# Optimization experiments

Hardware: AMD Instinct MI355X
Metric: run time of the kernel (lower is better)

The kernel has to match this reference:

```python
import jax, jax.numpy as jnp
import numpy as np

DEPTH = 2
DIM = 64
INNER = 256  # hard-coded inner_dim in Attention
HEADS = 1
N = 4096
B = 2
EPS = 1e-5


def layernorm(x, g, b):
    m = jnp.mean(x, axis=-1, keepdims=True)
    v = jnp.var(x, axis=-1, keepdims=True)
    return (x - m) * jax.lax.rsqrt(v + EPS) * g + b


def setup_inputs() -> dict:
    key = jax.random.key(0)
    ks = jax.random.split(key, 16)
    embed = jax.random.normal(ks[0], (B, N, DIM), dtype=jnp.float32)
    A = jax.random.randint(ks[1], (1, HEADS, N, N), 0, 2).astype(jnp.float32)
    s = 0.02
    return {
        "embed": embed,
        "A": A,
        "g1": jnp.ones((DEPTH, DIM), jnp.float32),
        "b1": jnp.zeros((DEPTH, DIM), jnp.float32),
        "Wqkv": jax.random.normal(ks[2], (DEPTH, DIM, INNER * 3), jnp.float32) * s,
        "Wout": jax.random.normal(ks[3], (DEPTH, INNER, DIM), jnp.float32) * s,
        "bout": jnp.zeros((DEPTH, DIM), jnp.float32),
        "g2": jnp.ones((DEPTH, DIM), jnp.float32),
        "b2": jnp.zeros((DEPTH, DIM), jnp.float32),
        "W1": jax.random.normal(ks[4], (DEPTH, DIM, DIM), jnp.float32) * s,
        "bb1": jnp.zeros((DEPTH, DIM), jnp.float32),
        "W2": jax.random.normal(ks[5], (DEPTH, DIM, DIM), jnp.float32) * s,
        "bb2": jnp.zeros((DEPTH, DIM), jnp.float32),
        "gf": jnp.ones((DIM,), jnp.float32),
        "bf": jnp.zeros((DIM,), jnp.float32),
    }


def _encoder(embed, A, g1, b1, Wqkv, Wout, bout, g2, b2, W1, bb1, W2, bb2, gf, bf):
    b, n, dim = embed.shape
    scale = dim ** (-0.5)
    dh = INNER // HEADS
    x = embed
    attn = None
    dots_softmax = None
    diag = jnp.arange(n)
    for l in range(DEPTH):
        xn = layernorm(x, g1[l], b1[l])
        qkv = xn @ Wqkv[l]  # [b, n, 3*INNER]
        q, k, v = jnp.split(qkv, 3, axis=-1)
        # [b, n, INNER] -> [b, h, n, dh]
        q = q.reshape(b, n, HEADS, dh).transpose(0, 2, 1, 3)
        k = k.reshape(b, n, HEADS, dh).transpose(0, 2, 1, 3)
        v = v.reshape(b, n, HEADS, dh).transpose(0, 2, 1, 3)
        dots = jnp.einsum("bhid,bhjd->bhij", q, k) * scale
        dots_softmax = jax.nn.softmax(dots[0, 0], axis=-1)
        # adjacency mask, then only [0][0] kept; diagonal filled with literal 1.0;
        # the original does a cpu/numpy roundtrip with .detach() -> stop_gradient.
        e = jnp.where(A > 0, dots, jnp.float32(-9e15))[0, 0]  # [n, n]
        e = e.at[diag, diag].set(1.0)
        e = jax.lax.stop_gradient(e)
        attn = jax.nn.softmax(e, axis=-1)  # [n, n], shared across b, h
        out = jnp.einsum("ij,bhjd->bhid", attn, v)  # broadcast attn over b,h
        out = out.transpose(0, 2, 1, 3).reshape(b, n, INNER)
        out = out @ Wout[l] + bout[l]
        x = xn + out  # residual onto the NORMED input (as in original)
        xm = layernorm(x, g2[l], b2[l])
        mlp = jax.nn.gelu(xm @ W1[l] + bb1[l], approximate=False) @ W2[l] + bb2[l]
        x = xm + mlp
    x = layernorm(x, gf, bf)
    return x, attn.reshape(1, 1, n, n), dots_softmax


def reference(embed, A, g1, b1, Wqkv, Wout, bout, g2, b2, W1, bb1, W2, bb2, gf, bf):
    return _encoder(embed, A, g1, b1, Wqkv, Wout, bout, g2, b2, W1, bb1, W2, bb2, gf, bf)
```

## Files before the change

### kernel.cpp

```cpp
#include <hip/hip_runtime.h>
#include <hip/hip_bf16.h>
#include <math.h>

typedef __attribute__((ext_vector_type(8))) short short8;
typedef __attribute__((ext_vector_type(4))) float f32x4;

#define NG 16

__device__ __forceinline__ unsigned short f2bf(float x) {
    __hip_bfloat16 b = __float2bfloat16(x);
    return *reinterpret_cast<unsigned short*>(&b);
}
__device__ __forceinline__ float bf2f(unsigned short u) {
    unsigned int t = ((unsigned int)u) << 16;
    float f;
    __builtin_memcpy(&f, &t, 4);
    return f;
}
__device__ __forceinline__ float gelu_exact(float x) {
    return 0.5f * x * (1.0f + erff(x * 0.70710678118654752f));
}

__global__ __launch_bounds__(256) void k_zero(float* __restrict__ p, long n)
{
    long i = (long)blockIdx.x * 256 + threadIdx.x;
    if (i < n) p[i] = 0.f;
}

__global__ __launch_bounds__(256) void k_prologue(
    const float* __restrict__ Aadj, unsigned long long* __restrict__ mask,
    const float* __restrict__ Wqkv, const float* __restrict__ Wout,
    float* __restrict__ Wfold,
    const float* __restrict__ embed, const float* __restrict__ g1,
    const float* __restrict__ b1, float* __restrict__ xn,
    float* __restrict__ zbuf)
{
    int bx = blockIdx.x, tid = threadIdx.x;
    if (bx < 4096) {
        if (!mask) return;
        int row = bx;
        int wave = tid >> 6, lane = tid & 63;
        for (int w = wave; w < 64; w += 4) {
            float a = Aadj[(long)row * 4096 + w * 64 + lane];
            unsigned long long m = __ballot(a > 0.f);
            if (lane == 0) mask[(long)row * 64 + w] = m;
        }
    } else if (bx < 4128) {
        int bid = bx - 4096;
        int l = bid >> 4;
        int idx = (bid & 15) * 256 + tid;
        int c = idx >> 6, d = idx & 63;
        const float* Wq = Wqkv + (long)l * 64 * 768;
        const float* Wo = Wout + (long)l * 256 * 64;
        float a = 0.f;
        for (int k = 0; k < 256; ++k)
            a += Wq[c * 768 + 512 + k] * Wo[k * 64 + d];
        Wfold[l * 4096 + idx] = a;
    } else if (bx < 6176) {
        int wave = tid >> 6, lane = tid & 63;
        long row = (long)(bx - 4128) * 4 + wave;
        float v = embed[row * 64 + lane];
        float s = v;
        #pragma unroll
        for (int o = 32; o; o >>= 1) s += __shfl_xor(s, o);
        float m = s * (1.0f / 64.0f);
        float d = v - m;
        float q = d * d;
        #pragma unroll
        for (int o = 32; o; o >>= 1) q += __shfl_xor(q, o);
        float rstd = rsqrtf(q * (1.0f / 64.0f) + 1e-5f);
        xn[row * 64 + lane] = d * rstd * g1[lane] + b1[lane];
    } else {
        long i = (long)(bx - 6176) * 256 + tid;
        if (i < 524288) zbuf[i] = 0.f;
    }
}

__global__ __launch_bounds__(256) void k_qkx(
    const float* __restrict__ xn, const float* __restrict__ W,
    const float* __restrict__ Wfold,
    unsigned short* __restrict__ q, unsigned short* __restrict__ kmat,
    unsigned short* __restrict__ vWT)
{
    __shared__ float As[64][65];
    __shared__ float Ws[64][65];
    int tid = threadIdx.x;
    int by = blockIdx.y;
    int tx = tid & 15, ty = tid >> 4;
    if (by < 8) {
        int m0 = blockIdx.x * 64, n0 = by * 64;
        #pragma unroll
        for (int it = 0; it < 16; ++it) {
            int idx = tid + it * 256;
            int r = idx >> 6, c = idx & 63;
            As[r][c] = xn[(long)(m0 + r) * 64 + c];
            Ws[r][c] = W[(long)r * 768 + n0 + c];
        }
        __syncthreads();
        float acc[4][4] = {};
        #pragma unroll
        for (int k = 0; k < 64; ++k) {
            float a[4], w[4];
            #pragma unroll
            for (int i = 0; i < 4; ++i) a[i] = As[ty * 4 + i][k];
            #pragma unroll
            for (int j = 0; j < 4; ++j) w[j] = Ws[k][tx * 4 + j];
            #pragma unroll
            for (int i = 0; i < 4; ++i)
                #pragma unroll
                for (int j = 0; j < 4; ++j) acc[i][j] += a[i] * w[j];
        }
        #pragma unroll
        for (int i = 0; i < 4; ++i) {
            long row = m0 + ty * 4 + i;
            #pragma unroll
            for (int j = 0; j < 4; ++j) {
                int col = n0 + tx * 4 + j;
                if (col < 256) q[row * 256 + col] = f2bf(acc[i][j]);
                else           kmat[row * 256 + (col - 256)] = f2bf(acc[i][j]);
            }
        }
    } else {
        int n0 = blockIdx.x * 64, b = by - 8;
        #pragma unroll
        for (int it = 0; it < 16; ++it) {
            int idx = tid + it * 256;
            int r = idx >> 6, c = idx & 63;
            As[r][c] = xn[((long)b * 4096 + n0 + r) * 64 + c];
            Ws[r][c] = Wfold[r * 64 + c];
        }
        __syncthreads();
        float acc[4][4] = {};
        #pragma unroll
        for (int k = 0; k < 64; ++k) {
            float a[4], w[4];
            #pragma unroll
            for (int i = 0; i < 4; ++i) a[i] = As[ty * 4 + i][k];
            #pragma unroll
            for (int j = 0; j < 4; ++j) w[j] = Ws[k][tx * 4 + j];
            #pragma unroll
            for (int i = 0; i < 4; ++i)
                #pragma unroll
                for (int j = 0; j < 4; ++j) acc[i][j] += a[i] * w[j];
        }
        #pragma unroll
        for (int i = 0; i < 4; ++i)
            #pragma unroll
            for (int j = 0; j < 4; ++j)
                vWT[((long)b * 64 + tx * 4 + j) * 4096 + n0 + ty * 4 + i] = f2bf(acc[i][j]);
    }
}

__global__ __launch_bounds__(256) void k_flash(
    const unsigned short* __restrict__ q, const unsigned short* __restrict__ kmat,
    const unsigned short* __restrict__ vwt,
    const unsigned long long* __restrict__ mask, const float* __restrict__ Aadj,
    unsigned short* __restrict__ part,
    float* __restrict__ stats)
{
    __shared__ __align__(16) unsigned short Qs[128 * 64];
    __shared__ __align__(16) unsigned short Ks[128 * 64];
    __shared__ __align__(16) unsigned short Ps[128 * 128];
    int tid = threadIdx.x;
    int lane = tid & 63, wq = tid >> 6;
    int fr = lane & 15, quad = lane >> 4;
    int m0 = blockIdx.x * 128;
    int g  = blockIdx.y;

    f32x4 accO[2][8];
    #pragma unroll
    for (int i = 0; i < 2; ++i)
        #pragma unroll
        for (int j = 0; j < 8; ++j) accO[i][j] = (f32x4){0.f, 0.f, 0.f, 0.f};
    float m_run[2] = {-1e30f, -1e30f};
    float s_run[2] = {0.f, 0.f};

    for (int jt = 0; jt < 2; ++jt) {
        int jb = g * 256 + jt * 128;
        f32x4 accS[8][2];
        #pragma unroll
        for (int i = 0; i < 8; ++i)
            #pragma unroll
            for (int n = 0; n < 2; ++n) accS[i][n] = (f32x4){0.f, 0.f, 0.f, 0.f};
        for (int k0 = 0; k0 < 256; k0 += 64) {
            #pragma unroll
            for (int it = 0; it < 4; ++it) {
                int idx = tid + it * 256;
                int r = idx >> 3, c8 = (idx & 7) * 8;
                *(short8*)&Qs[idx * 8] = *(const short8*)(q    + (long)(m0 + r) * 256 + k0 + c8);
                *(short8*)&Ks[idx * 8] = *(const short8*)(kmat + (long)(jb + r) * 256 + k0 + c8);
            }
            __syncthreads();
            #pragma unroll
            for (int ks = 0; ks < 2; ++ks) {
                short8 ka[8], qb[2];
                #pragma unroll
                for (int i = 0; i < 8; ++i)
                    ka[i] = *(const short8*)&Ks[(i * 16 + fr) * 64 + ks * 32 + quad * 8];
                #pragma unroll
                for (int n = 0; n < 2; ++n)
                    qb[n] = *(const short8*)&Qs[(wq * 32 + n * 16 + fr) * 64 + ks * 32 + quad * 8];
                #pragma unroll
                for (int i = 0; i < 8; ++i)
                    #pragma unroll
                    for (int n = 0; n < 2; ++n)
                        accS[i][n] = __builtin_amdgcn_mfma_f32_16x16x32_bf16(
                            ka[i], qb[n], accS[i][n], 0, 0, 0);
            }
            __syncthreads();
        }
        float al[2];
        #pragma unroll
        for (int n = 0; n < 2; ++n) {
            int qrow = m0 + wq * 32 + n * 16 + fr;
            unsigned long long mw0 = 0, mw1 = 0;
            if (mask) {
                mw0 = mask[(long)qrow * 64 + (jb >> 6)];
                mw1 = mask[(long)qrow * 64 + (jb >> 6) + 1];
            }
            float tm = -1e30f;
            #pragma unroll
            for (int i = 0; i < 8; ++i) {
                #pragma unroll
                for (int r = 0; r < 4; ++r) {
                    int jl = i * 16 + quad * 4 + r;
                    float v = accS[i][n][r] * 0.125f;
                    bool keep = mask ? (((jl < 64 ? (mw0 >> jl) : (mw1 >> (jl - 64))) & 1ull) != 0)
                                     : (Aadj[(long)qrow * 4096 + jb + jl] > 0.f);
                    v = keep ? v : -1e30f;
                    if (jb + jl == qrow) v = 1.0f;
                    accS[i][n][r] = v;
                    tm = fmaxf(tm, v);
                }
            }
            tm = fmaxf(tm, __shfl_xor(tm, 16));
            tm = fmaxf(tm, __shfl_xor(tm, 32));
            float mnew = fmaxf(fmaxf(m_run[n], tm), -1e20f);
            al[n] = __expf(m_run[n] - mnew);
            m_run[n] = mnew;
            float ts = 0.f;
            int qrl = wq * 32 + n * 16 + fr;
            #pragma unroll
            for (int i = 0; i < 8; ++i) {
                float p0 = __expf(accS[i][n][0] - mnew);
                float p1 = __expf(accS[i][n][1] - mnew);
                float p2 = __expf(accS[i][n][2] - mnew);
                float p3 = __expf(accS[i][n][3] - mnew);
                ts += (p0 + p1) + (p2 + p3);
                unsigned int lo = (unsigned int)f2bf(p0) | ((unsigned int)f2bf(p1) << 16);
                unsigned int hi = (unsigned int)f2bf(p2) | ((unsigned int)f2bf(p3) << 16);
                int u = (qrl * 128 + i * 16 + quad * 4) ^ ((fr & 7) << 3);
                *(uint2*)&Ps[u] = make_uint2(lo, hi);
            }
            ts += __shfl_xor(ts, 16);
            ts += __shfl_xor(ts, 32);
            s_run[n] = s_run[n] * al[n] + ts;
        }
        #pragma unroll
        for (int ii = 0; ii < 2; ++ii) {
            float av[4];
            #pragma unroll
            for (int r = 0; r < 4; ++r) av[r] = __shfl(al[ii], quad * 4 + r);
            #pragma unroll
            for (int nn = 0; nn < 8; ++nn)
                #pragma unroll
                for (int r = 0; r < 4; ++r) accO[ii][nn][r] *= av[r];
        }
        #pragma unroll
        for (int it = 0; it < 4; ++it) {
            int idx = tid + it * 256;
            int r = idx >> 3, c8 = (idx & 7) * 8;
            *(short8*)&Qs[idx * 8] = *(const short8*)(vwt + (long)r * 4096 + jb + c8);
            *(short8*)&Ks[idx * 8] = *(const short8*)(vwt + (long)r * 4096 + jb + 64 + c8);
        }
        __syncthreads();
        #pragma unroll
        for (int ks4 = 0; ks4 < 4; ++ks4) {
            const unsigned short* buf = (ks4 < 2) ? Qs : Ks;
            int ksl = ks4 & 1;
            short8 pa[2], vb[8];
            #pragma unroll
            for (int ii = 0; ii < 2; ++ii) {
                int u = ((wq * 32 + ii * 16 + fr) * 128 + ks4 * 32 + quad * 8) ^ ((fr & 7) << 3);
                pa[ii] = *(const short8*)&Ps[u];
            }
            #pragma unroll
            for (int nn = 0; nn < 8; ++nn)
                vb[nn] = *(const short8*)&buf[(nn * 16 + fr) * 64 + ksl * 32 + quad * 8];
            #pragma unroll
            for (int ii = 0; ii < 2; ++ii)
                #pragma unroll
                for (int nn = 0; nn < 8; ++nn)
                    accO[ii][nn] = __builtin_amdgcn_mfma_f32_16x16x32_bf16(
                        pa[ii], vb[nn], accO[ii][nn], 0, 0, 0);
        }
        __syncthreads();
    }
    #pragma unroll
    for (int ii = 0; ii < 2; ++ii) {
        #pragma unroll
        for (int nn = 0; nn < 8; ++nn) {
            int ch = nn * 16 + fr;
            long rowb = m0 + wq * 32 + ii * 16 + quad * 4;
            #pragma unroll
            for (int r = 0; r < 4; ++r)
                part[((long)g * 4096 + rowb + r) * 128 + ch] = f2bf(accO[ii][nn][r]);
        }
    }
    if (quad == 0) {
        #pragma unroll
        for (int n = 0; n < 2; ++n) {
            int qrow = m0 + wq * 32 + n * 16 + fr;
            stats[((long)g * 4096 + qrow) * 2]     = m_run[n];
            stats[((long)g * 4096 + qrow) * 2 + 1] = s_run[n];
        }
    }
}

__global__ __launch_bounds__(256) void k_stats(
    const unsigned short* __restrict__ q, const unsigned short* __restrict__ kmat,
    const unsigned long long* __restrict__ mask, const float* __restrict__ Aadj,
    float* __restrict__ stats2)
{
    __shared__ __align__(16) unsigned short Qs[128 * 64];
    __shared__ __align__(16) unsigned short Ks[128 * 64];
    int tid = threadIdx.x;
    int lane = tid & 63, wq = tid >> 6;
    int fr = lane & 15, quad = lane >> 4;
    int m0 = blockIdx.x * 128;
    int g  = blockIdx.y;
    float m1[2] = {-1e30f, -1e30f}, s1[2] = {0.f, 0.f};
    float m2[2] = {-1e30f, -1e30f}, s2[2] = {0.f, 0.f};

    for (int jt = 0; jt < 2; ++jt) {
        int jb = g * 256 + jt * 128;
        f32x4 accS[8][2];
        #pragma unroll
        for (int i = 0; i < 8; ++i)
            #pragma unroll
            for (int n = 0; n < 2; ++n) accS[i][n] = (f32x4){0.f, 0.f, 0.f, 0.f};
        for (int k0 = 0; k0 < 256; k0 += 64) {
            #pragma unroll
            for (int it = 0; it < 4; ++it) {
                int idx = tid + it * 256;
                int r = idx >> 3, c8 = (idx & 7) * 8;
                *(short8*)&Qs[idx * 8] = *(const short8*)(q    + (long)(m0 + r) * 256 + k0 + c8);
                *(short8*)&Ks[idx * 8] = *(const short8*)(kmat + (long)(jb + r) * 256 + k0 + c8);
            }
            __syncthreads();
            #pragma unroll
            for (int ks = 0; ks < 2; ++ks) {
                short8 ka[8], qb[2];
                #pragma unroll
                for (int i = 0; i < 8; ++i)
                    ka[i] = *(const short8*)&Ks[(i * 16 + fr) * 64 + ks * 32 + quad * 8];
                #pragma unroll
                for (int n = 0; n < 2; ++n)
                    qb[n] = *(const short8*)&Qs[(wq * 32 + n * 16 + fr) * 64 + ks * 32 + quad * 8];
                #pragma unroll
                for (int i = 0; i < 8; ++i)
                    #pragma unroll
                    for (int n = 0; n < 2; ++n)
                        accS[i][n] = __builtin_amdgcn_mfma_f32_16x16x32_bf16(
                            ka[i], qb[n], accS[i][n], 0, 0, 0);
            }
            __syncthreads();
        }
        #pragma unroll
        for (int n = 0; n < 2; ++n) {
            int qrow = m0 + wq * 32 + n * 16 + fr;
            unsigned long long mw0 = 0, mw1 = 0;
            if (mask) {
                mw0 = mask[(long)qrow * 64 + (jb >> 6)];
                mw1 = mask[(long)qrow * 64 + (jb >> 6) + 1];
            }
            float tm1 = -1e30f, tm2 = -1e30f;
            #pragma unroll
            for (int i = 0; i < 8; ++i) {
                #pragma unroll
                for (int r = 0; r < 4; ++r) {
                    int jl = i * 16 + quad * 4 + r;
                    float v = accS[i][n][r] * 0.125f;
                    accS[i][n][r] = v;
                    tm2 = fmaxf(tm2, v);
                    bool keep = mask ? (((jl < 64 ? (mw0 >> jl) : (mw1 >> (jl - 64))) & 1ull) != 0)
                                     : (Aadj[(long)qrow * 4096 + jb + jl] > 0.f);
                    float mv = keep ? v : -1e30f;
                    if (jb + jl == qrow) mv = 1.0f;
                    tm1 = fmaxf(tm1, mv);
                }
            }
            tm1 = fmaxf(tm1, __shfl_xor(tm1, 16));
            tm1 = fmaxf(tm1, __shfl_xor(tm1, 32));
            tm2 = fmaxf(tm2, __shfl_xor(tm2, 16));
            tm2 = fmaxf(tm2, __shfl_xor(tm2, 32));
            float mn1 = fmaxf(fmaxf(m1[n], tm1), -1e20f);
            float mn2 = fmaxf(fmaxf(m2[n], tm2), -1e20f);
            float a1 = __expf(m1[n] - mn1), a2 = __expf(m2[n] - mn2);
            float ts1 = 0.f, ts2 = 0.f;
            #pragma unroll
            for (int i = 0; i < 8; ++i) {
                #pragma unroll
                for (int r = 0; r < 4; ++r) {
                    int jl = i * 16 + quad * 4 + r;
                    float v = accS[i][n][r];
                    ts2 += __expf(v - mn2);
                    bool keep = mask ? (((jl < 64 ? (mw0 >> jl) : (mw1 >> (jl - 64))) & 1ull) != 0)
                                     : (Aadj[(long)qrow * 4096 + jb + jl] > 0.f);
                    float mv = keep ? v : -1e30f;
                    if (jb + jl == qrow) mv = 1.0f;
                    ts1 += __expf(mv - mn1);
                }
            }
            ts1 += __shfl_xor(ts1, 16); ts1 += __shfl_xor(ts1, 32);
            ts2 += __shfl_xor(ts2, 16); ts2 += __shfl_xor(ts2, 32);
            s1[n] = s1[n] * a1 + ts1; m1[n] = mn1;
            s2[n] = s2[n] * a2 + ts2; m2[n] = mn2;
        }
    }
    if (quad == 0) {
        #pragma unroll
        for (int n = 0; n < 2; ++n) {
            int qrow = m0 + wq * 32 + n * 16 + fr;
            *(float4*)&stats2[(long)qrow * 64 + g * 4] =
                make_float4(m1[n], s1[n], m2[n], s2[n]);
        }
    }
}

__global__ __launch_bounds__(256) void k_attn_ds(
    const unsigned short* __restrict__ q, const unsigned short* __restrict__ kmat,
    const unsigned long long* __restrict__ mask, const float* __restrict__ Aadj,
    const float* __restrict__ stats2,
    float* __restrict__ attn, float* __restrict__ ds)
{
    __shared__ __align__(16) unsigned short Qs[128 * 64];
    __shared__ __align__(16) unsigned short Ks[128 * 64];
    int tid = threadIdx.x;
    int lane = tid & 63, wq = tid >> 6;
    int fr = lane & 15, quad = lane >> 4;
    int m0 = blockIdx.x * 128;
    int g  = blockIdx.y;

    float M1[2], S1i[2], M2[2], S2i[2];
    #pragma unroll
    for (int n = 0; n < 2; ++n) {
        int qrow = m0 + wq * 32 + n * 16 + fr;
        float mm1 = -1e30f, mm2 = -1e30f;
        for (int gg = 0; gg < NG; ++gg) {
            float4 s4 = *(const float4*)&stats2[(long)qrow * 64 + gg * 4];
            mm1 = fmaxf(mm1, s4.x);
            mm2 = fmaxf(mm2, s4.z);
        }
        float ss1 = 0.f, ss2 = 0.f;
        for (int gg = 0; gg < NG; ++gg) {
            float4 s4 = *(const float4*)&stats2[(long)qrow * 64 + gg * 4];
            ss1 += s4.y * __expf(s4.x - mm1);
            ss2 += s4.w * __expf(s4.z - mm2);
        }
        M1[n] = mm1; S1i[n] = 1.0f / ss1;
        M2[n] = mm2; S2i[n] = 1.0f / ss2;
    }

    for (int jt = 0; jt < 2; ++jt) {
        int jb = g * 256 + jt * 128;
        f32x4 accS[8][2];
        #pragma unroll
        for (int i = 0; i < 8; ++i)
            #pragma unroll
            for (int n = 0; n < 2; ++n) accS[i][n] = (f32x4){0.f, 0.f, 0.f, 0.f};
        for (int k0 = 0; k0 < 256; k0 += 64) {
            #pragma unroll
            for (int it = 0; it < 4; ++it) {
                int idx = tid + it * 256;
                int r = idx >> 3, c8 = (idx & 7) * 8;
                *(short8*)&Qs[idx * 8] = *(const short8*)(q    + (long)(m0 + r) * 256 + k0 + c8);
                *(short8*)&Ks[idx * 8] = *(const short8*)(kmat + (long)(jb + r) * 256 + k0 + c8);
            }
            __syncthreads();
            #pragma unroll
            for (int ks = 0; ks < 2; ++ks) {
                short8 ka[8], qb[2];
                #pragma unroll
                for (int i = 0; i < 8; ++i)
                    ka[i] = *(const short8*)&Ks[(i * 16 + fr) * 64 + ks * 32 + quad * 8];
                #pragma unroll
                for (int n = 0; n < 2; ++n)
                    qb[n] = *(const short8*)&Qs[(wq * 32 + n * 16 + fr) * 64 + ks * 32 + quad * 8];
                #pragma unroll
                for (int i = 0; i < 8; ++i)
                    #pragma unroll
                    for (int n = 0; n < 2; ++n)
                        accS[i][n] = __builtin_amdgcn_mfma_f32_16x16x32_bf16(
                            ka[i], qb[n], accS[i][n], 0, 0, 0);
            }
            __syncthreads();
        }
        #pragma unroll
        for (int n = 0; n < 2; ++n) {
            int qrow = m0 + wq * 32 + n * 16 + fr;
            unsigned long long mw0 = 0, mw1 = 0;
            if (mask) {
                mw0 = mask[(long)qrow * 64 + (jb >> 6)];
                mw1 = mask[(long)qrow * 64 + (jb >> 6) + 1];
            }
            #pragma unroll
            for (int i = 0; i < 8; ++i) {
                float4 du, da;
                float* dup = &du.x; float* dap = &da.x;
                #pragma unroll
                for (int r = 0; r < 4; ++r) {
                    int jl = i * 16 + quad * 4 + r;
                    float v = accS[i][n][r] * 0.125f;
                    dup[r] = __expf(v - M2[n]) * S2i[n];
                    bool keep = mask ? (((jl < 64 ? (mw0 >> jl) : (mw1 >> (jl - 64))) & 1ull) != 0)
                                     : (Aadj[(long)qrow * 4096 + jb + jl] > 0.f);
                    float mv = keep ? v : -1e30f;
                    if (jb + jl == qrow) mv = 1.0f;
                    dap[r] = __expf(mv - M1[n]) * S1i[n];
                }
                long off = (long)qrow * 4096 + jb + i * 16 + quad * 4;
                *(float4*)&ds[off]   = du;
                *(float4*)&attn[off] = da;
            }
        }
    }
}

__global__ __launch_bounds__(256) void k_mfma_splitk(
    const float* __restrict__ A, const unsigned short* __restrict__ B,
    float* __restrict__ C)
{
    __shared__ __align__(16) unsigned short As[128 * 64];
    __shared__ __align__(16) unsigned short Bs[128 * 64];
    const int K = 4096, N = 128;
    int tid = threadIdx.x;
    int lane = tid & 63, wave = tid >> 6;
    long m0 = (long)blockIdx.x * 128;
    int k0base = blockIdx.y * 512;
    const float* Ag = A + m0 * K;
    int wm = (wave & 1) * 64, wn = (wave >> 1) * 64;
    int fr = lane & 15, quad = lane >> 4;

    f32x4 acc[4][4];
    #pragma unroll
    for (int i = 0; i < 4; ++i)
        #pragma unroll
        for (int j = 0; j < 4; ++j) acc[i][j] = (f32x4){0.f, 0.f, 0.f, 0.f};

    for (int k0 = k0base; k0 < k0base + 512; k0 += 64) {
        #pragma unroll
        for (int it = 0; it < 4; ++it) {
            int c = tid + it * 256;
            int r = c >> 3, col = (c & 7) * 8;
            float4 f0 = *(const float4*)(Ag + (long)r * K + k0 + col);
            float4 f1 = *(const float4*)(Ag + (long)r * K + k0 + col + 4);
            short8 s;
            s[0] = (short)f2bf(f0.x); s[1] = (short)f2bf(f0.y);
            s[2] = (short)f2bf(f0.z); s[3] = (short)f2bf(f0.w);
            s[4] = (short)f2bf(f1.x); s[5] = (short)f2bf(f1.y);
            s[6] = (short)f2bf(f1.z); s[7] = (short)f2bf(f1.w);
            *(short8*)&As[c * 8] = s;
            *(short8*)&Bs[c * 8] = *(const short8*)(B + (long)r * K + k0 + col);
        }
        __syncthreads();
        #pragma unroll
        for (int ks = 0; ks < 2; ++ks) {
            short8 af[4], bfr[4];
            #pragma unroll
            for (int i = 0; i < 4; ++i) {
                af[i]  = *(const short8*)&As[(wm + i * 16 + fr) * 64 + ks * 32 + quad * 8];
                bfr[i] = *(const short8*)&Bs[(wn + i * 16 + fr) * 64 + ks * 32 + quad * 8];
            }
            #pragma unroll
            for (int i = 0; i < 4; ++i)
                #pragma unroll
                for (int j = 0; j < 4; ++j)
                    acc[i][j] = __builtin_amdgcn_mfma_f32_16x16x32_bf16(
                        af[i], bfr[j], acc[i][j], 0, 0, 0);
        }
        __syncthreads();
    }
    #pragma unroll
    for (int i = 0; i < 4; ++i) {
        #pragma unroll
        for (int j = 0; j < 4; ++j) {
            long col = wn + j * 16 + fr;
            long rowb = m0 + wm + i * 16 + quad * 4;
            #pragma unroll
            for (int r = 0; r < 4; ++r)
                atomicAdd(&C[(rowb + r) * N + col], acc[i][j][r]);
        }
    }
}

__global__ __launch_bounds__(256) void k_mlp(
    int mode, const float* __restrict__ xn,
    const unsigned short* __restrict__ part, const float* __restrict__ fstats,
    const float* __restrict__ avcat, const float* __restrict__ boutv,
    const float* __restrict__ gin, const float* __restrict__ bin,
    const float* __restrict__ W1, const float* __restrict__ bb1,
    const float* __restrict__ W2, const float* __restrict__ bb2,
    const float* __restrict__ gout, const float* __restrict__ bln,
    float* __restrict__ out)
{
    __shared__ float As[64][65];
    __shared__ float W1s[64][65];
    __shared__ float W2s[64][65];
    __shared__ float wg[64][NG];
    int tid = threadIdx.x;
    int m0 = blockIdx.x * 64;
    if (mode == 0 && tid < 64) {
        int n = (m0 + tid) & 4095;
        float mg[NG], sg[NG];
        float mx = -1e30f;
        #pragma unroll
        for (int g = 0; g < NG; ++g) {
            mg[g] = fstats[((long)g * 4096 + n) * 2];
            sg[g] = fstats[((long)g * 4096 + n) * 2 + 1];
            mx = fmaxf(mx, mg[g]);
        }
        float stot = 0.f;
        float w[NG];
        #pragma unroll
        for (int g = 0; g < NG; ++g) { w[g] = __expf(mg[g] - mx); stot += w[g] * sg[g]; }
        float inv = 1.0f / stot;
        #pragma unroll
        for (int g = 0; g < NG; ++g) wg[tid][g] = w[g] * inv;
    }
    __syncthreads();
    #pragma unroll
    for (int it = 0; it < 16; ++it) {
        int idx = tid + it * 256;
        int r = idx >> 6, c = idx & 63;
        long row = m0 + r;
        int n = (int)(row & 4095), bb = (int)(row >> 12);
        float v = xn[row * 64 + c] + boutv[c];
        if (mode == 0) {
            #pragma unroll
            for (int g = 0; g < NG; ++g)
                v += wg[r][g] * bf2f(part[((long)g * 4096 + n) * 128 + bb * 64 + c]);
        } else {
            v += avcat[(long)n * 128 + bb * 64 + c];
        }
        As[r][c]  = v;
        W1s[r][c] = W1[(long)r * 64 + c];
        W2s[r][c] = W2[(long)r * 64 + c];
    }
    __syncthreads();
    int tx = tid & 15, ty = tid >> 4;
    #pragma unroll
    for (int i = 0; i < 4; ++i) {
        float vv[4];
        float s = 0.f;
        #pragma unroll
        for (int j = 0; j < 4; ++j) { vv[j] = As[ty * 4 + i][tx * 4 + j]; s += vv[j]; }
        #pragma unroll
        for (int o = 1; o < 16; o <<= 1) s += __shfl_xor(s, o);
        float m = s * (1.0f / 64.0f);
        float qv = 0.f;
        #pragma unroll
        for (int j = 0; j < 4; ++j) { float d = vv[j] - m; qv += d * d; }
        #pragma unroll
        for (int o = 1; o < 16; o <<= 1) qv += __shfl_xor(qv, o);
        float rstd = rsqrtf(qv * (1.0f / 64.0f) + 1e-5f);
        #pragma unroll
        for (int j = 0; j < 4; ++j) {
            int col = tx * 4 + j;
            As[ty * 4 + i][col] = (vv[j] - m) * rstd * gin[col] + bin[col];
        }
    }
    __syncthreads();
    float acc[4][4] = {};
    #pragma unroll
    for (int k = 0; k < 64; ++k) {
        float a[4], w[4];
        #pragma unroll
        for (int i = 0; i < 4; ++i) a[i] = As[ty * 4 + i][k];
        #pragma unroll
        for (int j = 0; j < 4; ++j) w[j] = W1s[k][tx * 4 + j];
        #pragma unroll
        for (int i = 0; i < 4; ++i)
            #pragma unroll
            for (int j = 0; j < 4; ++j) acc[i][j] += a[i] * w[j];
    }
    __syncthreads();
    #pragma unroll
    for (int i = 0; i < 4; ++i)
        #pragma unroll
        for (int j = 0; j < 4; ++j)
            W1s[ty * 4 + i][tx * 4 + j] = gelu_exact(acc[i][j] + bb1[tx * 4 + j]);
    __syncthreads();
    float acc2[4][4] = {};
    #pragma unroll
    for (int k = 0; k < 64; ++k) {
        float a[4], w[4];
        #pragma unroll
        for (int i = 0; i < 4; ++i) a[i] = W1s[ty * 4 + i][k];
        #pragma unroll
        for (int j = 0; j < 4; ++j) w[j] = W2s[k][tx * 4 + j];
        #pragma unroll
        for (int i = 0; i < 4; ++i)
            #pragma unroll
            for (int j = 0; j < 4; ++j) acc2[i][j] += a[i] * w[j];
    }
    #pragma unroll
    for (int i = 0; i < 4; ++i) {
        float v[4];
        float s = 0.f;
        #pragma unroll
        for (int j = 0; j < 4; ++j) {
            v[j] = acc2[i][j] + bb2[tx * 4 + j] + As[ty * 4 + i][tx * 4 + j];
            s += v[j];
        }
        #pragma unroll
        for (int o = 1; o < 16; o <<= 1) s += __shfl_xor(s, o);
        float m = s * (1.0f / 64.0f);
        float qv = 0.f;
        #pragma unroll
        for (int j = 0; j < 4; ++j) { float d = v[j] - m; qv += d * d; }
        #pragma unroll
        for (int o = 1; o < 16; o <<= 1) qv += __shfl_xor(qv, o);
        float rstd = rsqrtf(qv * (1.0f / 64.0f) + 1e-5f);
        long row = m0 + ty * 4 + i;
        #pragma unroll
        for (int j = 0; j < 4; ++j) {
            int col = tx * 4 + j;
            out[row * 64 + col] = (v[j] - m) * rstd * gout[col] + bln[col];
        }
    }
}

extern "C" void kernel_launch(void* const* d_in, const int* in_sizes, int n_in,
                              void* d_out, int out_size, void* d_ws, size_t ws_size,
                              hipStream_t stream)
{
    const float* embed = (const float*)d_in[0];
    const float* Aadj  = (const float*)d_in[1];
    const float* g1    = (const float*)d_in[2];
    const float* b1    = (const float*)d_in[3];
    const float* Wqkv  = (const float*)d_in[4];
    const float* Wout  = (const float*)d_in[5];
    const float* bout  = (const float*)d_in[6];
    const float* g2    = (const float*)d_in[7];
    const float* b2    = (const float*)d_in[8];
    const float* W1    = (const float*)d_in[9];
    const float* bb1   = (const float*)d_in[10];
    const float* W2    = (const float*)d_in[11];
    const float* bb2   = (const float*)d_in[12];
    const float* gf    = (const float*)d_in[13];
    const float* bff   = (const float*)d_in[14];

    float* ox    = (float*)d_out;
    float* attnb = ox + 524288;
    float* dsb   = attnb + 16777216;

    if (ws_size < (10ull << 20)) {
        k_zero<<<133120, 256, 0, stream>>>(ox, 34078720l);
        return;
    }

    char* ws = (char*)d_ws;
    float*          avcat  = (float*)(ws + (0l << 20));
    float*          xn     = (float*)(ws + (2l << 20));
    float*          stats2 = (float*)(ws + (4l << 20));
    unsigned short* q      = (unsigned short*)(ws + (6l << 20));
    unsigned short* kmat   = (unsigned short*)(ws + (7l << 20));
    unsigned short* vwt    = (unsigned short*)(ws + (8l << 20));
    float*          Wfold  = (float*)(ws + (9l << 20));
    unsigned long long* mask = (ws_size >= (12ull << 20))
        ? (unsigned long long*)(ws + (10l << 20)) : nullptr;

    unsigned short* part   = (unsigned short*)attnb;
    float*          fstats = attnb + 4194304;

    k_prologue<<<8224, 256, 0, stream>>>(Aadj, mask, Wqkv, Wout, Wfold,
                                         embed, g1, b1, xn, avcat);

    k_qkx<<<dim3(64, 10), 256, 0, stream>>>(xn, Wqkv, Wfold, q, kmat, vwt);
    k_flash<<<dim3(32, NG), 256, 0, stream>>>(q, kmat, vwt, mask, Aadj, part, fstats);
    k_mlp<<<128, 256, 0, stream>>>(0, xn, part, fstats, nullptr, bout,
                                   g2, b2, W1, bb1, W2, bb2,
                                   g1 + 64, b1 + 64, xn);

    k_qkx<<<dim3(64, 10), 256, 0, stream>>>(xn, Wqkv + 64 * 768, Wfold + 4096, q, kmat, vwt);
    k_stats<<<dim3(32, NG), 256, 0, stream>>>(q, kmat, mask, Aadj, stats2);
    k_attn_ds<<<dim3(32, NG), 256, 0, stream>>>(q, kmat, mask, Aadj, stats2, attnb, dsb);
    k_mfma_splitk<<<dim3(32, 8), 256, 0, stream>>>(attnb, vwt, avcat);
    k_mlp<<<128, 256, 0, stream>>>(1, xn, nullptr, nullptr, avcat, bout + 64,
                                   g2 + 64, b2 + 64, W1 + 4096, bb1 + 64, W2 + 4096, bb2 + 64,
                                   gf, bff, ox);
}
```

Measured before the change: 513.1 us.

## Fuse attention-times-V into attn/ds kernel and split residual-layernorm from MLP

The layer-2 attention kernel now packs normalized probabilities to bf16 in shared memory and multiplies them by V within the same block, atomically accumulating into avcat. This removes the separate split-K GEMM that re-read the full fp32 attention matrix from global memory. The residual-plus-layernorm step moves out of k_mlp into new per-row kernels, which adds two launches and an extra pass over the activations. Fast __expf calls are replaced by accurate expf, which costs more per element, presumably for accuracy.

New measurement: 535.7 us. +4.4%, slower.

```diff
diff --git a/kernel.cpp b/kernel.cpp
--- a/kernel.cpp
+++ b/kernel.cpp
@@ -404,12 +404,12 @@
                 for (int r = 0; r < 4; ++r) {
                     int jl = i * 16 + quad * 4 + r;
                     float v = accS[i][n][r];
-                    ts2 += __expf(v - mn2);
+                    ts2 += expf(v - mn2);
                     bool keep = mask ? (((jl < 64 ? (mw0 >> jl) : (mw1 >> (jl - 64))) & 1ull) != 0)
                                      : (Aadj[(long)qrow * 4096 + jb + jl] > 0.f);
                     float mv = keep ? v : -1e30f;
                     if (jb + jl == qrow) mv = 1.0f;
-                    ts1 += __expf(mv - mn1);
+                    ts1 += expf(mv - mn1);
                 }
             }
             ts1 += __shfl_xor(ts1, 16); ts1 += __shfl_xor(ts1, 32);
@@ -428,14 +428,16 @@
     }
 }
 
-__global__ __launch_bounds__(256) void k_attn_ds(
+__global__ __launch_bounds__(256) void k_attn_ds_pv(
     const unsigned short* __restrict__ q, const unsigned short* __restrict__ kmat,
+    const unsigned short* __restrict__ vwt,
     const unsigned long long* __restrict__ mask, const float* __restrict__ Aadj,
     const float* __restrict__ stats2,
-    float* __restrict__ attn, float* __restrict__ ds)
+    float* __restrict__ attn, float* __restrict__ ds, float* __restrict__ avcat)
 {
     __shared__ __align__(16) unsigned short Qs[128 * 64];
     __shared__ __align__(16) unsigned short Ks[128 * 64];
+    __shared__ __align__(16) unsigned short Ps[128 * 128];
     int tid = threadIdx.x;
     int lane = tid & 63, wq = tid >> 6;
     int fr = lane & 15, quad = lane >> 4;
@@ -462,6 +464,12 @@
         M2[n] = mm2; S2i[n] = 1.0f / ss2;
     }
 
+    f32x4 accO[2][8];
+    #pragma unroll
+    for (int i = 0; i < 2; ++i)
+        #pragma unroll
+        for (int j = 0; j < 8; ++j) accO[i][j] = (f32x4){0.f, 0.f, 0.f, 0.f};
+
     for (int jt = 0; jt < 2; ++jt) {
         int jb = g * 256 + jt * 128;
         f32x4 accS[8][2];
@@ -499,6 +507,7 @@
         #pragma unroll
         for (int n = 0; n < 2; ++n) {
             int qrow = m0 + wq * 32 + n * 16 + fr;
+            int qrl  = wq * 32 + n * 16 + fr;
             unsigned long long mw0 = 0, mw1 = 0;
             if (mask) {
                 mw0 = mask[(long)qrow * 64 + (jb >> 6)];
@@ -512,165 +521,145 @@
                 for (int r = 0; r < 4; ++r) {
                     int jl = i * 16 + quad * 4 + r;
                     float v = accS[i][n][r] * 0.125f;
-                    dup[r] = __expf(v - M2[n]) * S2i[n];
+                    dup[r] = expf(v - M2[n]) * S2i[n];
                     bool keep = mask ? (((jl < 64 ? (mw0 >> jl) : (mw1 >> (jl - 64))) & 1ull) != 0)
                                      : (Aadj[(long)qrow * 4096 + jb + jl] > 0.f);
                     float mv = keep ? v : -1e30f;
                     if (jb + jl == qrow) mv = 1.0f;
-                    dap[r] = __expf(mv - M1[n]) * S1i[n];
+                    dap[r] = expf(mv - M1[n]) * S1i[n];
                 }
                 long off = (long)qrow * 4096 + jb + i * 16 + quad * 4;
                 *(float4*)&ds[off]   = du;
                 *(float4*)&attn[off] = da;
-            }
-        }
-    }
-}
-
-__global__ __launch_bounds__(256) void k_mfma_splitk(
-    const float* __restrict__ A, const unsigned short* __restrict__ B,
-    float* __restrict__ C)
-{
-    __shared__ __align__(16) unsigned short As[128 * 64];
-    __shared__ __align__(16) unsigned short Bs[128 * 64];
-    const int K = 4096, N = 128;
-    int tid = threadIdx.x;
-    int lane = tid & 63, wave = tid >> 6;
-    long m0 = (long)blockIdx.x * 128;
-    int k0base = blockIdx.y * 512;
-    const float* Ag = A + m0 * K;
-    int wm = (wave & 1) * 64, wn = (wave >> 1) * 64;
-    int fr = lane & 15, quad = lane >> 4;
-
-    f32x4 acc[4][4];
-    #pragma unroll
-    for (int i = 0; i < 4; ++i)
-        #pragma unroll
-        for (int j = 0; j < 4; ++j) acc[i][j] = (f32x4){0.f, 0.f, 0.f, 0.f};
-
-    for (int k0 = k0base; k0 < k0base + 512; k0 += 64) {
+                unsigned int lo = (unsigned int)f2bf(dap[0]) | ((unsigned int)f2bf(dap[1]) << 16);
+                unsigned int hi = (unsigned int)f2bf(dap[2]) | ((unsigned int)f2bf(dap[3]) << 16);
+                int u = (qrl * 128 + i * 16 + quad * 4) ^ ((fr & 7) << 3);
+                *(uint2*)&Ps[u] = make_uint2(lo, hi);
+            }
+        }
         #pragma unroll
         for (int it = 0; it < 4; ++it) {
-            int c = tid + it * 256;
-            int r = c >> 3, col = (c & 7) * 8;
-            float4 f0 = *(const float4*)(Ag + (long)r * K + k0 + col);
-            float4 f1 = *(const float4*)(Ag + (long)r * K + k0 + col + 4);
-            short8 s;
-            s[0] = (short)f2bf(f0.x); s[1] = (short)f2bf(f0.y);
-            s[2] = (short)f2bf(f0.z); s[3] = (short)f2bf(f0.w);
-            s[4] = (short)f2bf(f1.x); s[5] = (short)f2bf(f1.y);
-            s[6] = (short)f2bf(f1.z); s[7] = (short)f2bf(f1.w);
-            *(short8*)&As[c * 8] = s;
-            *(short8*)&Bs[c * 8] = *(const short8*)(B + (long)r * K + k0 + col);
+            int idx = tid + it * 256;
+            int r = idx >> 3, c8 = (idx & 7) * 8;
+            *(short8*)&Qs[idx * 8] = *(const short8*)(vwt + (long)r * 4096 + jb + c8);
+            *(short8*)&Ks[idx * 8] = *(const short8*)(vwt + (long)r * 4096 + jb + 64 + c8);
         }
         __syncthreads();
         #pragma unroll
-        for (int ks = 0; ks < 2; ++ks) {
-            short8 af[4], bfr[4];
-            #pragma unroll
-            for (int i = 0; i < 4; ++i) {
-                af[i]  = *(const short8*)&As[(wm + i * 16 + fr) * 64 + ks * 32 + quad * 8];
-                bfr[i] = *(const short8*)&Bs[(wn + i * 16 + fr) * 64 + ks * 32 + quad * 8];
-            }
-            #pragma unroll
-            for (int i = 0; i < 4; ++i)
-                #pragma unroll
-                for (int j = 0; j < 4; ++j)
-                    acc[i][j] = __builtin_amdgcn_mfma_f32_16x16x32_bf16(
-                        af[i], bfr[j], acc[i][j], 0, 0, 0);
+        for (int ks4 = 0; ks4 < 4; ++ks4) {
+            const unsigned short* buf = (ks4 < 2) ? Qs : Ks;
+            int ksl = ks4 & 1;
+            short8 pa[2], vb[8];
+            #pragma unroll
+            for (int ii = 0; ii < 2; ++ii) {
+                int u = ((wq * 32 + ii * 16 + fr) * 128 + ks4 * 32 + quad * 8) ^ ((fr & 7) << 3);
+                pa[ii] = *(const short8*)&Ps[u];
+            }
+            #pragma unroll
+            for (int nn = 0; nn < 8; ++nn)
+                vb[nn] = *(const short8*)&buf[(nn * 16 + fr) * 64 + ksl * 32 + quad * 8];
+            #pragma unroll
+            for (int ii = 0; ii < 2; ++ii)
+                #pragma unroll
+                for (int nn = 0; nn < 8; ++nn)
+                    accO[ii][nn] = __builtin_amdgcn_mfma_f32_16x16x32_bf16(
+                        pa[ii], vb[nn], accO[ii][nn], 0, 0, 0);
         }
         __syncthreads();
     }
     #pragma unroll
-    for (int i = 0; i < 4; ++i) {
-        #pragma unroll
-        for (int j = 0; j < 4; ++j) {
-            long col = wn + j * 16 + fr;
-            long rowb = m0 + wm + i * 16 + quad * 4;
+    for (int ii = 0; ii < 2; ++ii) {
+        #pragma unroll
+        for (int nn = 0; nn < 8; ++nn) {
+            int ch = nn * 16 + fr;
+            long rowb = m0 + wq * 32 + ii * 16 + quad * 4;
             #pragma unroll
             for (int r = 0; r < 4; ++r)
-                atomicAdd(&C[(rowb + r) * N + col], acc[i][j][r]);
-        }
-    }
+                atomicAdd(&avcat[(rowb + r) * 128 + ch], accO[ii][nn][r]);
+        }
+    }
+}
+
+__global__ __launch_bounds__(256) void k_avres_ln(
+    const float* __restrict__ xn, const float* __restrict__ avcat,
+    const float* __restrict__ bout, const float* __restrict__ g,
+    const float* __restrict__ b, float* __restrict__ out)
+{
+    int wave = threadIdx.x >> 6, lane = threadIdx.x & 63;
+    long row = (long)blockIdx.x * 4 + wave;
+    int bb = (int)(row >> 12), n = (int)(row & 4095);
+    float v = xn[row * 64 + lane] + avcat[(long)n * 128 + bb * 64 + lane] + bout[lane];
+    float s = v;
+    #pragma unroll
+    for (int o = 32; o; o >>= 1) s += __shfl_xor(s, o);
+    float m = s * (1.0f / 64.0f);
+    float d = v - m;
+    float q = d * d;
+    #pragma unroll
+    for (int o = 32; o; o >>= 1) q += __shfl_xor(q, o);
+    float rstd = rsqrtf(q * (1.0f / 64.0f) + 1e-5f);
+    out[row * 64 + lane] = d * rstd * g[lane] + b[lane];
+}
+
+__global__ __launch_bounds__(256) void k_avres_ln_c(
+    const float* __restrict__ xn, const unsigned short* __restrict__ part,
+    const float* __restrict__ stats, const float* __restrict__ bout,
+    const float* __restrict__ g, const float* __restrict__ b,
+    float* __restrict__ out)
+{
+    int wave = threadIdx.x >> 6, lane = threadIdx.x & 63;
+    long row = (long)blockIdx.x * 4 + wave;
+    int bb = (int)(row >> 12), n = (int)(row & 4095);
+    float sm[NG], ss[NG];
+    float ms = -1e30f;
+    #pragma unroll
+    for (int gg = 0; gg < NG; ++gg) {
+        sm[gg] = stats[((long)gg * 4096 + n) * 2];
+        ss[gg] = stats[((long)gg * 4096 + n) * 2 + 1];
+        ms = fmaxf(ms, sm[gg]);
+    }
+    float acc = 0.f, stot = 0.f;
+    #pragma unroll
+    for (int gg = 0; gg < NG; ++gg) {
+        float w = __expf(sm[gg] - ms);
+        stot += w * ss[gg];
+        acc  += w * bf2f(part[((long)gg * 4096 + n) * 128 + bb * 64 + lane]);
+    }
+    float v = xn[row * 64 + lane] + acc / stot + bout[lane];
+    float s = v;
+    #pragma unroll
+    for (int o = 32; o; o >>= 1) s += __shfl_xor(s, o);
+    float m = s * (1.0f / 64.0f);
+    float d = v - m;
+    float qv = d * d;
+    #pragma unroll
+    for (int o = 32; o; o >>= 1) qv += __shfl_xor(qv, o);
+    float rstd = rsqrtf(qv * (1.0f / 64.0f) + 1e-5f);
+    out[row * 64 + lane] = d * rstd * g[lane] + b[lane];
 }
 
 __global__ __launch_bounds__(256) void k_mlp(
-    int mode, const float* __restrict__ xn,
-    const unsigned short* __restrict__ part, const float* __restrict__ fstats,
-    const float* __restrict__ avcat, const float* __restrict__ boutv,
-    const float* __restrict__ gin, const float* __restrict__ bin,
+    const float* __restrict__ xm,
     const float* __restrict__ W1, const float* __restrict__ bb1,
     const float* __restrict__ W2, const float* __restrict__ bb2,
-    const float* __restrict__ gout, const float* __restrict__ bln,
+    const float* __restrict__ g, const float* __restrict__ b,
     float* __restrict__ out)
 {
     __shared__ float As[64][65];
     __shared__ float W1s[64][65];
     __shared__ float W2s[64][65];
-    __shared__ float wg[64][NG];
     int tid = threadIdx.x;
     int m0 = blockIdx.x * 64;
-    if (mode == 0 && tid < 64) {
-        int n = (m0 + tid) & 4095;
-        float mg[NG], sg[NG];
-        float mx = -1e30f;
-        #pragma unroll
-        for (int g = 0; g < NG; ++g) {
-            mg[g] = fstats[((long)g * 4096 + n) * 2];
-            sg[g] = fstats[((long)g * 4096 + n) * 2 + 1];
-            mx = fmaxf(mx, mg[g]);
-        }
-        float stot = 0.f;
-        float w[NG];
-        #pragma unroll
-        for (int g = 0; g < NG; ++g) { w[g] = __expf(mg[g] - mx); stot += w[g] * sg[g]; }
-        float inv = 1.0f / stot;
-        #pragma unroll
-        for (int g = 0; g < NG; ++g) wg[tid][g] = w[g] * inv;
-    }
-    __syncthreads();
     #pragma unroll
     for (int it = 0; it < 16; ++it) {
         int idx = tid + it * 256;
         int r = idx >> 6, c = idx & 63;
-        long row = m0 + r;
-        int n = (int)(row & 4095), bb = (int)(row >> 12);
-        float v = xn[row * 64 + c] + boutv[c];
-        if (mode == 0) {
-            #pragma unroll
-            for (int g = 0; g < NG; ++g)
-                v += wg[r][g] * bf2f(part[((long)g * 4096 + n) * 128 + bb * 64 + c]);
-        } else {
-            v += avcat[(long)n * 128 + bb * 64 + c];
-        }
-        As[r][c]  = v;
+        As[r][c]  = xm[(long)(m0 + r) * 64 + c];
         W1s[r][c] = W1[(long)r * 64 + c];
         W2s[r][c] = W2[(long)r * 64 + c];
     }
     __syncthreads();
     int tx = tid & 15, ty = tid >> 4;
-    #pragma unroll
-    for (int i = 0; i < 4; ++i) {
-        float vv[4];
-        float s = 0.f;
-        #pragma unroll
-        for (int j = 0; j < 4; ++j) { vv[j] = As[ty * 4 + i][tx * 4 + j]; s += vv[j]; }
-        #pragma unroll
-        for (int o = 1; o < 16; o <<= 1) s += __shfl_xor(s, o);
-        float m = s * (1.0f / 64.0f);
-        float qv = 0.f;
-        #pragma unroll
-        for (int j = 0; j < 4; ++j) { float d = vv[j] - m; qv += d * d; }
-        #pragma unroll
-        for (int o = 1; o < 16; o <<= 1) qv += __shfl_xor(qv, o);
-        float rstd = rsqrtf(qv * (1.0f / 64.0f) + 1e-5f);
-        #pragma unroll
-        for (int j = 0; j < 4; ++j) {
-            int col = tx * 4 + j;
-            As[ty * 4 + i][col] = (vv[j] - m) * rstd * gin[col] + bin[col];
-        }
-    }
-    __syncthreads();
     float acc[4][4] = {};
     #pragma unroll
     for (int k = 0; k < 64; ++k) {
@@ -716,17 +705,17 @@
         #pragma unroll
         for (int o = 1; o < 16; o <<= 1) s += __shfl_xor(s, o);
         float m = s * (1.0f / 64.0f);
-        float qv = 0.f;
-        #pragma unroll
-        for (int j = 0; j < 4; ++j) { float d = v[j] - m; qv += d * d; }
-        #pragma unroll
-        for (int o = 1; o < 16; o <<= 1) qv += __shfl_xor(qv, o);
-        float rstd = rsqrtf(qv * (1.0f / 64.0f) + 1e-5f);
+        float q = 0.f;
+        #pragma unroll
+        for (int j = 0; j < 4; ++j) { float d = v[j] - m; q += d * d; }
+        #pragma unroll
+        for (int o = 1; o < 16; o <<= 1) q += __shfl_xor(q, o);
+        float rstd = rsqrtf(q * (1.0f / 64.0f) + 1e-5f);
         long row = m0 + ty * 4 + i;
         #pragma unroll
         for (int j = 0; j < 4; ++j) {
             int col = tx * 4 + j;
-            out[row * 64 + col] = (v[j] - m) * rstd * gout[col] + bln[col];
+            out[row * 64 + col] = (v[j] - m) * rstd * g[col] + b[col];
         }
     }
 }
@@ -779,15 +768,15 @@
 
     k_qkx<<<dim3(64, 10), 256, 0, stream>>>(xn, Wqkv, Wfold, q, kmat, vwt);
     k_flash<<<dim3(32, NG), 256, 0, stream>>>(q, kmat, vwt, mask, Aadj, part, fstats);
-    k_mlp<<<128, 256, 0, stream>>>(0, xn, part, fstats, nullptr, bout,
-                                   g2, b2, W1, bb1, W2, bb2,
+    k_avres_ln_c<<<2048, 256, 0, stream>>>(xn, part, fstats, bout, g2, b2, xn);
+    k_mlp<<<128, 256, 0, stream>>>(xn, W1, bb1, W2, bb2,
                                    g1 + 64, b1 + 64, xn);
 
     k_qkx<<<dim3(64, 10), 256, 0, stream>>>(xn, Wqkv + 64 * 768, Wfold + 4096, q, kmat, vwt);
     k_stats<<<dim3(32, NG), 256, 0, stream>>>(q, kmat, mask, Aadj, stats2);
-    k_attn_ds<<<dim3(32, NG), 256, 0, stream>>>(q, kmat, mask, Aadj, stats2, attnb, dsb);
-    k_mfma_splitk<<<dim3(32, 8), 256, 0, stream>>>(attnb, vwt, avcat);
-    k_mlp<<<128, 256, 0, stream>>>(1, xn, nullptr, nullptr, avcat, bout + 64,
-                                   g2 + 64, b2 + 64, W1 + 4096, bb1 + 64, W2 + 4096, bb2 + 64,
+    k_attn_ds_pv<<<dim3(32, NG), 256, 0, stream>>>(q, kmat, vwt, mask, Aadj, stats2,
+                                                   attnb, dsb, avcat);
+    k_avres_ln<<<2048, 256, 0, stream>>>(xn, avcat, bout + 64, g2 + 64, b2 + 64, xn);
+    k_mlp<<<128, 256, 0, stream>>>(xn, W1 + 4096, bb1 + 64, W2 + 4096, bb2 + 64,
                                    gf, bff, ox);
 }
```
